# Kernel tuning notes

Hardware: AMD Instinct MI355X
Metric: run time of the kernel (lower is better)

The kernel has to match this reference:

```python
import jax, jax.numpy as jnp
import numpy as np

N = 100000          # n_nodes
E = 1600000         # n_edges (avg degree 16)
IN = 256            # in_dim
OUT = 16            # out_dim
SLOPE = 0.2         # leaky_relu negative slope
DROP = 0.5          # dropout rate


def _xavier(key, shape):
    fan_in, fan_out = shape
    std = (2.0 / (fan_in + fan_out)) ** 0.5
    return std * jax.random.normal(key, shape, jnp.float32)


def setup_inputs() -> dict:
    key = jax.random.key(0)
    ks = jax.random.split(key, 10)
    x = jax.random.normal(ks[0], (N, IN), jnp.float32)
    row = jax.random.randint(ks[1], (E,), 0, N, jnp.int32)
    col = jax.random.randint(ks[2], (E,), 0, N, jnp.int32)
    edge_w = jax.random.uniform(ks[3], (E,), jnp.float32)
    W1 = _xavier(ks[4], (IN, IN // 2)); b1 = jnp.zeros((IN // 2,), jnp.float32)
    W2 = _xavier(ks[5], (IN // 2, IN // 4)); b2 = jnp.zeros((IN // 4,), jnp.float32)
    W3 = _xavier(ks[6], (IN // 4, IN // 8)); b3 = jnp.zeros((IN // 8,), jnp.float32)
    W4 = _xavier(ks[7], (IN // 8, OUT)); b4 = jnp.zeros((OUT,), jnp.float32)
    # dropout mask (training-mode dropout made deterministic; pre-scaled by 1/(1-p))
    drop_mask = (jax.random.uniform(ks[8], (N, IN // 2)) > DROP).astype(jnp.float32) / (1.0 - DROP)
    return dict(x=x, row=row, col=col, edge_w=edge_w,
                W1=W1, b1=b1, W2=W2, b2=b2, W3=W3, b3=b3, W4=W4, b4=b4,
                drop_mask=drop_mask)


def reference(x, row, col, edge_w, W1, b1, W2, b2, W3, b3, W4, b4, drop_mask):
    def spmm(h):
        # out[i] = sum over edges (i <- j): w_ij * h[j]   (sparse adj @ h)
        return jax.ops.segment_sum(edge_w[:, None] * h[col], row, num_segments=N)

    lrelu = lambda v: jax.nn.leaky_relu(v, SLOPE)

    h = spmm(x @ W1) + b1          # gc1: [N, IN/2]
    h = lrelu(h) * drop_mask       # leaky_relu + dropout
    h = spmm(h @ W2) + b2          # gc2: [N, IN/4]
    h = lrelu(h)
    h = lrelu(h @ W3 + b3)         # clf hidden: [N, IN/8]
    return h @ W4 + b4             # logits: [N, OUT]
```

## Files before the change

### kernel.cpp

```cpp
#include <hip/hip_runtime.h>
#include <hip/hip_bf16.h>

#define N_NODES 100000
#define N_EDGES 1600000
#define SLOPE_ 0.2f
#define NBK 196
#define BCAP 9216
#define NCB 13
#define KEYS (512 * NCB)
#define BINBLK 256

typedef __attribute__((ext_vector_type(8))) short bf16x8;
typedef __attribute__((ext_vector_type(4))) float f32x4;

__device__ __forceinline__ short f2bf(float f) {
    __hip_bfloat16 h = __float2bfloat16(f);
    return *reinterpret_cast<short*>(&h);
}
__device__ __forceinline__ float bflo(unsigned u) { return __uint_as_float(u << 16); }
__device__ __forceinline__ float bfhi(unsigned u) { return __uint_as_float(u & 0xFFFF0000u); }
__device__ __forceinline__ float bf2f(short s) {
    return __uint_as_float(((unsigned)(unsigned short)s) << 16);
}


__global__ void passA_k(const int* __restrict__ row, const int* __restrict__ col,
                        const float* __restrict__ ew, int* __restrict__ cur,
                        int2* __restrict__ binned) {
    __shared__ int hist[NBK], base[NBK], off[NBK];
    int t = threadIdx.x;
    const int chunk = N_EDGES / BINBLK;
    int e0 = blockIdx.x * chunk;
    for (int i = t; i < NBK; i += 256) { hist[i] = 0; off[i] = 0; }
    __syncthreads();
    for (int i = t; i < chunk; i += 256) {
        int b = row[e0 + i] >> 9;
        atomicAdd(&hist[b], 1);
    }
    __syncthreads();
    for (int i = t; i < NBK; i += 256)
        base[i] = atomicAdd(&cur[i], hist[i]);
    __syncthreads();
    for (int i = t; i < chunk; i += 256) {
        int e = e0 + i;
        int r = row[e], c = col[e];
        int b = r >> 9;
        int p = base[b] + atomicAdd(&off[b], 1);
        if (p < BCAP)
            binned[(size_t)b * BCAP + p] =
                make_int2(((r & 511) << 17) | c, __float_as_int(ew[e]));
    }
}


__global__ void __launch_bounds__(512) passB_k(const int2* __restrict__ binned,
                                               const int* __restrict__ cur,
                                               unsigned* __restrict__ cw,
                                               int* __restrict__ row_ptr) {
    __shared__ int hist[KEYS];
    __shared__ int offs[KEYS];
    __shared__ int ssum[512];
    __shared__ int bexc[256];
    int t = threadIdx.x, b = blockIdx.x;
    const int2* src = binned + (size_t)b * BCAP;
    int cnt = cur[b];
    if (cnt > BCAP) cnt = BCAP;

    if (t < 256) bexc[t] = (t < NBK) ? min(cur[t], BCAP) : 0;
    __syncthreads();
    for (int off2 = 1; off2 < 256; off2 <<= 1) {
        int v = (t < 256 && t >= off2) ? bexc[t - off2] : 0;
        __syncthreads();
        if (t < 256) bexc[t] += v;
        __syncthreads();
    }
    int gbase = bexc[b] - cnt;

    for (int i = t; i < KEYS; i += 512) hist[i] = 0;
    __syncthreads();

    for (int i = t; i < cnt; i += 512) {
        int2 v = src[i];
        int c = v.x & 0x1FFFF, lr = v.x >> 17;
        atomicAdd(&hist[lr * NCB + (c >> 13)], 1);
    }
    __syncthreads();

    int loc[NCB];
    int tot = 0;
#pragma unroll
    for (int j = 0; j < NCB; j++) {
        loc[j] = tot;
        tot += hist[t * NCB + j];
    }
    ssum[t] = tot;
    __syncthreads();
    for (int off2 = 1; off2 < 512; off2 <<= 1) {
        int v = (t >= off2) ? ssum[t - off2] : 0;
        __syncthreads();
        ssum[t] += v;
        __syncthreads();
    }
    int base = ssum[t] - tot;
#pragma unroll
    for (int j = 0; j < NCB; j++) offs[t * NCB + j] = base + loc[j];

    int grow = b * 512 + t;
    if (grow <= N_NODES) row_ptr[grow] = gbase + base;
    __syncthreads();

    for (int i = t; i < cnt; i += 512) {
        int2 v = src[i];
        int c = v.x & 0x1FFFF, lr = v.x >> 17;
        int p = gbase + atomicAdd(&offs[lr * NCB + (c >> 13)], 1);
        unsigned wb = (unsigned)(unsigned short)f2bf(__int_as_float(v.y));
        cw[p] = ((unsigned)c << 15) | (wb & 0x7FFFu);
    }
}


__global__ void prep_k(const float* __restrict__ W1, const float* __restrict__ W2,
                       const float* __restrict__ mask,
                       short* __restrict__ Bp1, short* __restrict__ Bp2,
                       unsigned* __restrict__ mp) {
    int i = blockIdx.x * 256 + threadIdx.x;
    if (i < 4096) {
        int ln = i & 15, nt = (i >> 4) & 7, g = (i >> 7) & 3, ks = i >> 9;
        int n = nt * 16 + ln, k0 = ks * 32 + g * 8;
        bf16x8 v;
#pragma unroll
        for (int j = 0; j < 8; j++) v[j] = f2bf(W1[(k0 + j) * 128 + n]);
        *(bf16x8*)(Bp1 + (size_t)i * 8) = v;
    } else if (i < 5120) {
        int c = i - 4096;
        int ln = c & 15, nt = (c >> 4) & 3, g = (c >> 6) & 3, ks = c >> 8;
        int n = nt * 16 + ln, k0 = ks * 32 + g * 8;
        bf16x8 v;
#pragma unroll
        for (int j = 0; j < 8; j++) v[j] = f2bf(W2[(k0 + j) * 64 + n]);
        *(bf16x8*)(Bp2 + (size_t)c * 8) = v;
    } else if (blockIdx.x >= 20) {
        int wi = i - 5120;
        if (wi < N_NODES * 4) {
            const float4* p = (const float4*)(mask + (size_t)wi * 32);
            unsigned b = 0;
#pragma unroll
            for (int j = 0; j < 8; j++) {
                float4 v = p[j];
                b |= (unsigned)(v.x != 0.f) << (4 * j);
                b |= (unsigned)(v.y != 0.f) << (4 * j + 1);
                b |= (unsigned)(v.z != 0.f) << (4 * j + 2);
                b |= (unsigned)(v.w != 0.f) << (4 * j + 3);
            }
            mp[wi] = b;
        }
    }
}


template <int K, int COLS, bool ABF16>
__global__ __launch_bounds__(512) void gemm_p(const void* __restrict__ Ap,
                                              const short* __restrict__ Bp,
                                              short* __restrict__ out, int M) {
    constexpr int NT = COLS / 16;
    constexpr int NKS = K / 32;
    __shared__ short Bs[K * COLS];
    int t = threadIdx.x;
    for (int i = t; i < K * COLS / 8; i += 512)
        *(bf16x8*)(Bs + (size_t)i * 8) = *(const bf16x8*)(Bp + (size_t)i * 8);
    __syncthreads();

    int l = t & 63, wv = t >> 6;
    int ln = l & 15, g = l >> 4;
    int row0 = blockIdx.x * 256 + wv * 32;
    int r0 = row0 + ln, r1 = row0 + 16 + ln;
    int cr0 = min(r0, M - 1), cr1 = min(r1, M - 1);

    f32x4 acc[2][NT];
#pragma unroll
    for (int rf = 0; rf < 2; rf++)
#pragma unroll
        for (int nt = 0; nt < NT; nt++) acc[rf][nt] = (f32x4){0.f, 0.f, 0.f, 0.f};

#pragma unroll
    for (int ks = 0; ks < NKS; ks++) {
        int kk = ks * 32 + g * 8;
        bf16x8 a0, a1;
        if constexpr (ABF16) {
            a0 = *(const bf16x8*)((const short*)Ap + (size_t)cr0 * K + kk);
            a1 = *(const bf16x8*)((const short*)Ap + (size_t)cr1 * K + kk);
        } else {
            const float* p0 = (const float*)Ap + (size_t)cr0 * K + kk;
            const float* p1 = (const float*)Ap + (size_t)cr1 * K + kk;
            float4 u0 = *(const float4*)p0;
            float4 u1 = *(const float4*)(p0 + 4);
            float4 v0 = *(const float4*)p1;
            float4 v1 = *(const float4*)(p1 + 4);
            a0[0] = f2bf(u0.x); a0[1] = f2bf(u0.y); a0[2] = f2bf(u0.z); a0[3] = f2bf(u0.w);
            a0[4] = f2bf(u1.x); a0[5] = f2bf(u1.y); a0[6] = f2bf(u1.z); a0[7] = f2bf(u1.w);
            a1[0] = f2bf(v0.x); a1[1] = f2bf(v0.y); a1[2] = f2bf(v0.z); a1[3] = f2bf(v0.w);
            a1[4] = f2bf(v1.x); a1[5] = f2bf(v1.y); a1[6] = f2bf(v1.z); a1[7] = f2bf(v1.w);
        }
#pragma unroll
        for (int nt = 0; nt < NT; nt++) {
            bf16x8 b = *(const bf16x8*)(Bs + (size_t)((((ks * 4 + g) * NT + nt) * 16 + ln)) * 8);
            acc[0][nt] = __builtin_amdgcn_mfma_f32_16x16x32_bf16(a0, b, acc[0][nt], 0, 0, 0);
            acc[1][nt] = __builtin_amdgcn_mfma_f32_16x16x32_bf16(a1, b, acc[1][nt], 0, 0, 0);
        }
    }
#pragma unroll
    for (int rf = 0; rf < 2; rf++)
#pragma unroll
        for (int nt = 0; nt < NT; nt++)
#pragma unroll
            for (int r = 0; r < 4; r++) {
                int orow = row0 + rf * 16 + g * 4 + r;
                if (orow < M) out[(size_t)orow * COLS + nt * 16 + ln] = f2bf(acc[rf][nt][r]);
            }
}


template <int D, bool DROP>
__global__ void spmm_bf(const int* __restrict__ row_ptr, const unsigned* __restrict__ cwp,
                        const short* __restrict__ h,
                        const float* __restrict__ bias, const unsigned* __restrict__ maskp,
                        short* __restrict__ out, int n) {
    int bid = blockIdx.x;
    int sbid = (bid & 7) * 3125 + (bid >> 3);
    int wid = sbid * 4 + (int)(threadIdx.x >> 6);
    int lane = threadIdx.x & 63;
    if (wid >= n) return;
    int sp = __builtin_amdgcn_readfirstlane(row_ptr[wid]);
    int ep = __builtin_amdgcn_readfirstlane(row_ptr[wid + 1]);
    int cnt = ep - sp;
    const unsigned* pcw = cwp + sp;
    const unsigned* hb = (const unsigned*)h;
    float ax = 0.f, ay = 0.f;

    if (D == 128) {
        for (int jb = 0; jb < cnt; jb += 8) {
            unsigned u[8];
            float w[8];
#pragma unroll
            for (int p = 0; p < 8; p++) {
                int idx = jb + p;
                unsigned md = pcw[idx];
                md = (idx < cnt) ? md : 0u;
                int c = (int)(md >> 15);
                w[p] = __uint_as_float((md & 0x7FFFu) << 16);
                u[p] = hb[(size_t)c * 64 + lane];
            }
#pragma unroll
            for (int p = 0; p < 8; p++) {
                ax += w[p] * bflo(u[p]);
                ay += w[p] * bfhi(u[p]);
            }
        }
        float2 b = *(const float2*)(bias + 2 * lane);
        float ox = ax + b.x, oy = ay + b.y;
        ox = ox > 0.f ? ox : SLOPE_ * ox;
        oy = oy > 0.f ? oy : SLOPE_ * oy;
        if (DROP) {
            unsigned mw = maskp[(size_t)wid * 4 + (lane >> 4)];
            unsigned sh = (2 * lane) & 31;
            ox = ((mw >> sh) & 1u) ? 2.f * ox : 0.f;
            oy = ((mw >> (sh + 1)) & 1u) ? 2.f * oy : 0.f;
        }
        unsigned ov = (unsigned)(unsigned short)f2bf(ox) |
                      ((unsigned)(unsigned short)f2bf(oy) << 16);
        *(unsigned*)(out + (size_t)wid * 128 + 2 * lane) = ov;
    } else {
        int li = lane & 31;
        for (int jb = 0; jb < cnt; jb += 8) {
            unsigned u[4];
            float w[4];
#pragma unroll
            for (int p = 0; p < 4; p++) {
                int iA = jb + 2 * p, iB = iA + 1;
                unsigned mA = pcw[iA];
                mA = (iA < cnt) ? mA : 0u;
                unsigned mB = pcw[iB];
                mB = (iB < cnt) ? mB : 0u;
                unsigned md = (lane < 32) ? mA : mB;
                int c = (int)(md >> 15);
                w[p] = __uint_as_float((md & 0x7FFFu) << 16);
                u[p] = hb[(size_t)c * 32 + li];
            }
#pragma unroll
            for (int p = 0; p < 4; p++) {
                ax += w[p] * bflo(u[p]);
                ay += w[p] * bfhi(u[p]);
            }
        }
        ax += __shfl_xor(ax, 32);
        ay += __shfl_xor(ay, 32);
        float2 b = *(const float2*)(bias + li * 2);
        float ox = ax + b.x, oy = ay + b.y;
        ox = ox > 0.f ? ox : SLOPE_ * ox;
        oy = oy > 0.f ? oy : SLOPE_ * oy;
        unsigned ov = (unsigned)(unsigned short)f2bf(ox) |
                      ((unsigned)(unsigned short)f2bf(oy) << 16);
        if (lane < 32) *(unsigned*)(out + (size_t)wid * 64 + li * 2) = ov;
    }
}


__global__ void clf_k(const short* __restrict__ h, const float* __restrict__ W3,
                      const float* __restrict__ b3, const float* __restrict__ W4,
                      const float* __restrict__ b4, float* __restrict__ out) {
    __shared__ float W3s[64][32];
    __shared__ float W4s[32][16];
    __shared__ float b3s[32], b4s[16];
    __shared__ float hs[32][64];
    __shared__ float t4[32][33];
    int t = threadIdx.x;
    for (int l = t; l < 64 * 32; l += 256) W3s[l / 32][l % 32] = W3[l];
    for (int l = t; l < 32 * 16; l += 256) W4s[l / 16][l % 16] = W4[l];
    if (t < 32) b3s[t] = b3[t];
    if (t < 16) b4s[t] = b4[t];
    int row0 = blockIdx.x * 32;
    {
        bf16x8 v = *(const bf16x8*)(h + (size_t)row0 * 64 + t * 8);
        int r = t >> 3, c0 = (t & 7) << 3;
#pragma unroll
        for (int j = 0; j < 8; j++) hs[r][c0 + j] = bf2f(v[j]);
    }
    __syncthreads();
    for (int l = t; l < 1024; l += 256) {
        int r = l / 32, c = l % 32;
        float a = b3s[c];
#pragma unroll 8
        for (int k = 0; k < 64; k++) a += hs[r][k] * W3s[k][c];
        t4[r][c] = a > 0.f ? a : SLOPE_ * a;
    }
    __syncthreads();
    for (int l = t; l < 512; l += 256) {
        int r = l / 16, c = l % 16;
        float a = b4s[c];
#pragma unroll
        for (int k = 0; k < 32; k++) a += t4[r][k] * W4s[k][c];
        out[(size_t)(row0 + r) * 16 + c] = a;
    }
}


extern "C" void kernel_launch(void* const* d_in, const int* in_sizes, int n_in,
                              void* d_out, int out_size, void* d_ws, size_t ws_size,
                              hipStream_t stream) {
    const float* x = (const float*)d_in[0];
    const int* row = (const int*)d_in[1];
    const int* col = (const int*)d_in[2];
    const float* ew = (const float*)d_in[3];
    const float* W1 = (const float*)d_in[4];
    const float* b1 = (const float*)d_in[5];
    const float* W2 = (const float*)d_in[6];
    const float* b2 = (const float*)d_in[7];
    const float* W3 = (const float*)d_in[8];
    const float* b3 = (const float*)d_in[9];
    const float* W4 = (const float*)d_in[10];
    const float* b4 = (const float*)d_in[11];
    const float* mask = (const float*)d_in[12];
    float* out = (float*)d_out;

    const int N = N_NODES, E = N_EDGES;

    short* h0 = (short*)d_ws;
    short* h1 = h0 + (size_t)N * 128;
    short* h2 = h1 + (size_t)N * 128;
    short* h3 = h2 + (size_t)N * 64;
    short* Bp1 = h3 + (size_t)N * 64;
    short* Bp2 = Bp1 + 32768;
    int* row_ptr = (int*)(Bp2 + 8192);
    int* cur = row_ptr + N + 1;
    unsigned* mask_p = (unsigned*)(cur + NBK + 3);
    unsigned* cwp = mask_p + (size_t)N * 4;
    int2* binned = (int2*)h0;

    hipMemsetAsync(cur, 0, NBK * sizeof(int), stream);
    passA_k<<<BINBLK, 256, 0, stream>>>(row, col, ew, cur, binned);
    passB_k<<<NBK, 512, 0, stream>>>(binned, cur, cwp, row_ptr);
    prep_k<<<1583, 256, 0, stream>>>(W1, W2, mask, Bp1, Bp2, mask_p);

    gemm_p<256, 128, false><<<(N + 255) / 256, 512, 0, stream>>>(x, Bp1, h0, N);
    spmm_bf<128, true><<<25000, 256, 0, stream>>>(row_ptr, cwp, h0, b1, mask_p, h1, N);
    gemm_p<128, 64, true><<<(N + 255) / 256, 512, 0, stream>>>(h1, Bp2, h2, N);
    spmm_bf<64, false><<<25000, 256, 0, stream>>>(row_ptr, cwp, h2, b2, nullptr, h3, N);
    clf_k<<<N / 32, 256, 0, stream>>>(h3, W3, b3, W4, b4, out);
}
```

Before: 237.4 us.

## Split edge binning into count/scan/scatter passes and fuse prep into count kernel

Replaces the single 256-block binning kernel, which used global atomics on bucket cursors, with a three-pass count, scan and scatter scheme over 1000 blocks. Per-block bucket offsets are computed deterministically, so the scatter kernel needs only shared-memory atomics. The weight-packing and dropout-mask packing are folded into the count kernel, and mask packing now uses wave ballots with coalesced loads. This raises parallelism in the preprocessing stage and removes a memset and a launch, at the cost of an extra scan kernel and a second pass over the row array.

Result: no change. 236.0 us (-0.6%).

```diff
diff --git a/kernel.cpp b/kernel.cpp
--- a/kernel.cpp
+++ b/kernel.cpp
@@ -8,7 +8,10 @@
 #define BCAP 9216
 #define NCB 13
 #define KEYS (512 * NCB)
-#define BINBLK 256
+#define BINBLK2 1000
+#define CHUNK2 1600
+#define PREPW 20
+#define PMBLK 1563
 
 typedef __attribute__((ext_vector_type(8))) short bf16x8;
 typedef __attribute__((ext_vector_type(4))) float f32x4;
@@ -24,28 +27,108 @@
 }
 
 
-__global__ void passA_k(const int* __restrict__ row, const int* __restrict__ col,
-                        const float* __restrict__ ew, int* __restrict__ cur,
-                        int2* __restrict__ binned) {
-    __shared__ int hist[NBK], base[NBK], off[NBK];
+__global__ void countA_k(const int* __restrict__ row, int* __restrict__ counts,
+                         const float* __restrict__ W1, const float* __restrict__ W2,
+                         const float* __restrict__ mask,
+                         short* __restrict__ Bp1, short* __restrict__ Bp2,
+                         unsigned* __restrict__ mp) {
     int t = threadIdx.x;
-    const int chunk = N_EDGES / BINBLK;
-    int e0 = blockIdx.x * chunk;
-    for (int i = t; i < NBK; i += 256) { hist[i] = 0; off[i] = 0; }
-    __syncthreads();
-    for (int i = t; i < chunk; i += 256) {
-        int b = row[e0 + i] >> 9;
-        atomicAdd(&hist[b], 1);
-    }
-    __syncthreads();
-    for (int i = t; i < NBK; i += 256)
-        base[i] = atomicAdd(&cur[i], hist[i]);
-    __syncthreads();
-    for (int i = t; i < chunk; i += 256) {
+    if (blockIdx.x < BINBLK2) {
+        __shared__ int hist[NBK];
+        for (int i = t; i < NBK; i += 256) hist[i] = 0;
+        __syncthreads();
+        int e0 = blockIdx.x * CHUNK2;
+        for (int i = t; i < CHUNK2; i += 256)
+            atomicAdd(&hist[row[e0 + i] >> 9], 1);
+        __syncthreads();
+        for (int i = t; i < NBK; i += 256)
+            counts[(size_t)i * BINBLK2 + blockIdx.x] = hist[i];
+        return;
+    }
+    int bi = blockIdx.x - BINBLK2;
+    if (bi < PREPW) {
+        int i = bi * 256 + t;
+        if (i < 4096) {
+            int ln = i & 15, nt = (i >> 4) & 7, g = (i >> 7) & 3, ks = i >> 9;
+            int n = nt * 16 + ln, k0 = ks * 32 + g * 8;
+            bf16x8 v;
+#pragma unroll
+            for (int j = 0; j < 8; j++) v[j] = f2bf(W1[(k0 + j) * 128 + n]);
+            *(bf16x8*)(Bp1 + (size_t)i * 8) = v;
+        } else if (i < 5120) {
+            int c = i - 4096;
+            int ln = c & 15, nt = (c >> 4) & 3, g = (c >> 6) & 3, ks = c >> 8;
+            int n = nt * 16 + ln, k0 = ks * 32 + g * 8;
+            bf16x8 v;
+#pragma unroll
+            for (int j = 0; j < 8; j++) v[j] = f2bf(W2[(k0 + j) * 64 + n]);
+            *(bf16x8*)(Bp2 + (size_t)c * 8) = v;
+        }
+        return;
+    }
+    int pb = bi - PREPW;
+    long fbase = (long)pb * 8192;
+    int wv = t >> 6, lane = t & 63;
+    const long FLIM = (long)N_NODES * 128;
+    for (int it = 0; it < 32; ++it) {
+        long f = fbase + it * 256 + wv * 64 + lane;
+        float v = (f < FLIM) ? mask[f] : 0.f;
+        unsigned long long bl = __ballot(v != 0.f);
+        if (lane == 0) {
+            long w = f >> 5;
+            if (w < (long)N_NODES * 4)
+                *(unsigned long long*)(mp + w) = bl;
+        }
+    }
+}
+
+
+__global__ void scanA_k(const int* __restrict__ counts, int* __restrict__ bases,
+                        int* __restrict__ cur) {
+    __shared__ int s[256];
+    int b = blockIdx.x, t = threadIdx.x;
+    const int* src = counts + (size_t)b * BINBLK2;
+    int v[4];
+    int loc = 0;
+#pragma unroll
+    for (int j = 0; j < 4; j++) {
+        int idx = t * 4 + j;
+        v[j] = (idx < BINBLK2) ? src[idx] : 0;
+        loc += v[j];
+    }
+    s[t] = loc;
+    __syncthreads();
+    for (int off = 1; off < 256; off <<= 1) {
+        int u = (t >= off) ? s[t - off] : 0;
+        __syncthreads();
+        s[t] += u;
+        __syncthreads();
+    }
+    int run = s[t] - loc;
+    int* dst = bases + (size_t)b * BINBLK2;
+#pragma unroll
+    for (int j = 0; j < 4; j++) {
+        int idx = t * 4 + j;
+        if (idx < BINBLK2) dst[idx] = run;
+        run += v[j];
+    }
+    if (t == 255) cur[b] = min(s[255], BCAP);
+}
+
+
+__global__ void scatterA_k(const int* __restrict__ row, const int* __restrict__ col,
+                           const float* __restrict__ ew, const int* __restrict__ bases,
+                           int2* __restrict__ binned) {
+    __shared__ int off[NBK];
+    int t = threadIdx.x, blk = blockIdx.x;
+    for (int i = t; i < NBK; i += 256) off[i] = bases[(size_t)i * BINBLK2 + blk];
+    __syncthreads();
+    int e0 = blk * CHUNK2;
+    for (int i = t; i < CHUNK2; i += 256) {
         int e = e0 + i;
         int r = row[e], c = col[e];
         int b = r >> 9;
-        int p = base[b] + atomicAdd(&off[b], 1);
+        int p = atomicAdd(&off[b], 1);
         if (p < BCAP)
             binned[(size_t)b * BCAP + p] =
                 make_int2(((r & 511) << 17) | c, __float_as_int(ew[e]));
@@ -115,45 +198,6 @@
         int p = gbase + atomicAdd(&offs[lr * NCB + (c >> 13)], 1);
         unsigned wb = (unsigned)(unsigned short)f2bf(__int_as_float(v.y));
         cw[p] = ((unsigned)c << 15) | (wb & 0x7FFFu);
-    }
-}
-
-
-__global__ void prep_k(const float* __restrict__ W1, const float* __restrict__ W2,
-                       const float* __restrict__ mask,
-                       short* __restrict__ Bp1, short* __restrict__ Bp2,
-                       unsigned* __restrict__ mp) {
-    int i = blockIdx.x * 256 + threadIdx.x;
-    if (i < 4096) {
-        int ln = i & 15, nt = (i >> 4) & 7, g = (i >> 7) & 3, ks = i >> 9;
-        int n = nt * 16 + ln, k0 = ks * 32 + g * 8;
-        bf16x8 v;
-#pragma unroll
-        for (int j = 0; j < 8; j++) v[j] = f2bf(W1[(k0 + j) * 128 + n]);
-        *(bf16x8*)(Bp1 + (size_t)i * 8) = v;
-    } else if (i < 5120) {
-        int c = i - 4096;
-        int ln = c & 15, nt = (c >> 4) & 3, g = (c >> 6) & 3, ks = c >> 8;
-        int n = nt * 16 + ln, k0 = ks * 32 + g * 8;
-        bf16x8 v;
-#pragma unroll
-        for (int j = 0; j < 8; j++) v[j] = f2bf(W2[(k0 + j) * 64 + n]);
-        *(bf16x8*)(Bp2 + (size_t)c * 8) = v;
-    } else if (blockIdx.x >= 20) {
-        int wi = i - 5120;
-        if (wi < N_NODES * 4) {
-            const float4* p = (const float4*)(mask + (size_t)wi * 32);
-            unsigned b = 0;
-#pragma unroll
-            for (int j = 0; j < 8; j++) {
-                float4 v = p[j];
-                b |= (unsigned)(v.x != 0.f) << (4 * j);
-                b |= (unsigned)(v.y != 0.f) << (4 * j + 1);
-                b |= (unsigned)(v.z != 0.f) << (4 * j + 2);
-                b |= (unsigned)(v.w != 0.f) << (4 * j + 3);
-            }
-            mp[wi] = b;
-        }
     }
 }
 
@@ -374,12 +418,15 @@
     int* cur = row_ptr + N + 1;
     unsigned* mask_p = (unsigned*)(cur + NBK + 3);
     unsigned* cwp = mask_p + (size_t)N * 4;
+    int* counts = (int*)(cwp + E + 16);
+    int* bases = counts + NBK * BINBLK2;
     int2* binned = (int2*)h0;
 
-    hipMemsetAsync(cur, 0, NBK * sizeof(int), stream);
-    passA_k<<<BINBLK, 256, 0, stream>>>(row, col, ew, cur, binned);
+    countA_k<<<BINBLK2 + PREPW + PMBLK, 256, 0, stream>>>(row, counts, W1, W2, mask,
+                                                          Bp1, Bp2, mask_p);
+    scanA_k<<<NBK, 256, 0, stream>>>(counts, bases, cur);
+    scatterA_k<<<BINBLK2, 256, 0, stream>>>(row, col, ew, bases, binned);
     passB_k<<<NBK, 512, 0, stream>>>(binned, cur, cwp, row_ptr);
-    prep_k<<<1583, 256, 0, stream>>>(W1, W2, mask, Bp1, Bp2, mask_p);
 
     gemm_p<256, 128, false><<<(N + 255) / 256, 512, 0, stream>>>(x, Bp1, h0, N);
     spmm_bf<128, true><<<25000, 256, 0, stream>>>(row_ptr, cwp, h0, b1, mask_p, h1, N);
```
